# Kernel tuning notes

Measured on AMD Instinct MI355X. Metric: run time of the kernel, lower is better.

Reference implementation:

```python
import jax, jax.numpy as jnp
import numpy as np

N, C, H, W = 32, 512, 56, 56
L, CT, HEAD, GROUPS = 64, 512, 16, 16
SIZE, POS_DIM = 14, 49  # PosEncoder(size=14, num_downsample=1) -> 14^2 // 4 = 49


def setup_inputs() -> dict:
    key = jax.random.key(0)
    ks = jax.random.split(key, 8)
    return {
        "feature": jax.random.normal(ks[0], (N, C, H, W), jnp.float32),
        "w_tc": jax.random.normal(ks[1], (L, C), jnp.float32) * 0.02,
        "b_tc": jnp.zeros((L,), jnp.float32),
        "w_val": jax.random.normal(ks[2], (GROUPS, CT // GROUPS, C // GROUPS), jnp.float32) * 0.02,
        "b_val": jnp.zeros((CT,), jnp.float32),
        "w_ds3": jax.random.normal(ks[3], (1, 1, 3, 3), jnp.float32) * 0.1,
        "b_ds3": jnp.zeros((1,), jnp.float32),
        "w_ds1": jax.random.normal(ks[4], (1, 1), jnp.float32) * 0.1,
        "b_ds1": jnp.zeros((1,), jnp.float32),
        "w_pos": jax.random.normal(ks[5], (POS_DIM, POS_DIM), jnp.float32) * 0.02,
        "b_pos": jnp.zeros((POS_DIM,), jnp.float32),
        "w_tok": jax.random.normal(ks[6], (CT, CT + POS_DIM), jnp.float32) * 0.02,
        "b_tok": jnp.zeros((CT,), jnp.float32),
    }


def reference(feature, w_tc, b_tc, w_val, b_val, w_ds3, b_ds3, w_ds1, b_ds1,
              w_pos, b_pos, w_tok, b_tok):
    n, c, h, w = feature.shape
    hw = h * w
    # --- static token coefficients: 1x1 conv C->L, scale, softmax over HW ---
    tc = jnp.einsum('nchw,lc->nlhw', feature, w_tc) + b_tc[None, :, None, None]
    tc = tc.reshape(n, 1, L, hw).transpose(0, 1, 3, 2) / np.sqrt(c)  # (N,1,HW,L)
    tc = jax.nn.softmax(tc, axis=2)
    # --- grouped 1x1 conv value: C -> CT (groups=16) ---
    fg = feature.reshape(n, GROUPS, c // GROUPS, hw)
    val = jnp.einsum('ngci,gdc->ngdi', fg, w_val).reshape(n, CT, hw) + b_val[None, :, None]
    val = val.reshape(n, HEAD, CT // HEAD, hw)
    # --- token aggregation: (N,h,CT/h,HW) @ (N,1,HW,L) -> (N,CT,L) ---
    tokens = jnp.matmul(val, tc).reshape(n, CT, -1)
    # --- PosEncoder: view coef maps as images, nearest-resize to 14x14 ---
    pc = tc.reshape(n * L, 1, h, w)  # torch .view memory reinterpretation
    ih = (jnp.arange(SIZE) * h) // SIZE
    iw = (jnp.arange(SIZE) * w) // SIZE
    pc = pc[:, :, ih][:, :, :, iw]  # (N*L,1,14,14) nearest interpolate
    # conv3x3 stride 2 pad 1: 14 -> 7
    pc = jax.lax.conv_general_dilated(pc, w_ds3, (2, 2), ((1, 1), (1, 1))) + b_ds3[None, :, None, None]
    # conv1x1 (1->1)
    pc = jnp.einsum('nchw,dc->ndhw', pc, w_ds1) + b_ds1[None, :, None, None]
    pc = pc.reshape(n, L, POS_DIM).transpose(0, 2, 1)  # (N,49,L)
    pos = jnp.einsum('ncl,dc->ndl', pc, w_pos) + b_pos[None, :, None]
    # --- concat + final 1x1 conv1d (CT+49 -> CT) ---
    tokens = jnp.concatenate([tokens, pos], axis=1)
    tokens = jnp.einsum('ncl,dc->ndl', tokens, w_tok) + b_tok[None, :, None]
    return tokens  # (N, CT, L)
```

## Files before the change

### kernel.cpp

```cpp
#include <hip/hip_runtime.h>
#include <hip/hip_bf16.h>
#include <cstddef>
#include <cstdint>

namespace {

constexpr int kN = 32;
constexpr int kC = 512;
constexpr int kHW = 3136;
constexpr int kL = 64;
constexpr int kCT = 512;
constexpr int kTok = 561;
constexpr int kKcat = 576;

typedef float fx4 __attribute__((ext_vector_type(4)));
typedef float f32x4 __attribute__((ext_vector_type(4)));
typedef short short8 __attribute__((ext_vector_type(8)));
typedef unsigned int u32x2 __attribute__((ext_vector_type(2)));

static __device__ inline unsigned short bf16_1(float x) {
  __hip_bfloat16 h = __float2bfloat16(x);
  unsigned short u;
  __builtin_memcpy(&u, &h, 2);
  return u;
}
static __device__ inline unsigned pk2(float a, float b) {
  __hip_bfloat162 h2 = __float22bfloat162_rn(make_float2(a, b));
  unsigned u;
  __builtin_memcpy(&u, &h2, 4);
  return u;
}
static __device__ inline float bf2f(unsigned short h) {
  unsigned u = (unsigned)h << 16;
  float f;
  __builtin_memcpy(&f, &u, 4);
  return f;
}

__global__ __launch_bounds__(256) void prep_kernel(
    const float* __restrict__ w_tok, const float* __restrict__ w_val,
    const float* __restrict__ b_val, const float* __restrict__ b_tok,
    const float* __restrict__ w_tc, unsigned short* __restrict__ wcat16,
    float* __restrict__ cst, unsigned short* __restrict__ wtc16,
    float* __restrict__ denom, unsigned short* __restrict__ bcat16) {
  int idx = blockIdx.x * 256 + threadIdx.x;
  if (idx < kCT * kKcat) {
    int d = idx / kKcat;
    int c = idx - d * kKcat;
    float v = 0.f;
    if (c < kCT) {
      int g = c >> 5, k = c & 31;
      const float* wt = w_tok + (size_t)d * kTok + g * 32;
      const float* wv = w_val + g * 1024 + k;
      float s = 0.f;
#pragma unroll
      for (int dp = 0; dp < 32; ++dp) s += wt[dp] * wv[dp * 32];
      v = s;
    } else if (c < kTok) {
      v = w_tok[(size_t)d * kTok + c];
    }
    wcat16[idx] = bf16_1(v);
    return;
  }
  idx -= kCT * kKcat;
  if (idx < kCT) {
    float s = b_tok[idx];
    for (int c = 0; c < kCT; ++c) s += w_tok[(size_t)idx * kTok + c] * b_val[c];
    cst[idx] = s;
    return;
  }
  idx -= kCT;
  if (idx < kL * kC) {
    wtc16[idx] = bf16_1(w_tc[idx]);
    return;
  }
  idx -= kL * kC;
  if (idx < kN * kL) {
    denom[idx] = 0.f;
    return;
  }
  idx -= kN * kL;
  if (idx < kN * kL * 15) {
    int n = idx / (kL * 15);
    int r = idx - n * (kL * 15);
    int l = r / 15;
    int k = kTok + (r - l * 15);
    bcat16[(size_t)n * kL * kKcat + (size_t)l * kKcat + k] = 0;
  }
}

__global__ __launch_bounds__(256) void tc_gemm2_kernel(
    const float* __restrict__ feat, const unsigned short* __restrict__ wtc16,
    const float* __restrict__ b_tc, unsigned short* __restrict__ expT,
    unsigned short* __restrict__ feat16, float* __restrict__ denom) {
  const int n = blockIdx.y;
  const int pb = blockIdx.x * 128;
  const int tid = threadIdx.x;
  const int wave = tid >> 6, lane = tid & 63;
  const int quad = lane >> 4, l16 = lane & 15;
  __shared__ unsigned short Bs[128][72];
  __shared__ float bsm[64];
  __shared__ float denom_s[64];
  if (tid < 64) {
    bsm[tid] = b_tc[tid];
    denom_s[tid] = 0.f;
  }

  f32x4 acc[4][2];
#pragma unroll
  for (int i = 0; i < 4; ++i)
#pragma unroll
    for (int j = 0; j < 2; ++j) acc[i][j] = (f32x4){0.f, 0.f, 0.f, 0.f};

  const float* fb = feat + (size_t)n * kC * kHW;
  unsigned short* f16b = feat16 + (size_t)n * kC * kHW;
  const int bc4 = (tid & 15) * 4, bpl0 = (tid >> 4) * 4;
  int pe_[2];
#pragma unroll
  for (int pass = 0; pass < 2; ++pass) {
    int pe = pb + bpl0 + pass * 64;
    pe_[pass] = pe < 3132 ? pe : 3132;
  }

  fx4 va[2][4], vb[2][4];
  auto LOADT = [&](int c0, fx4 (&v)[2][4]) {
#pragma unroll
    for (int pass = 0; pass < 2; ++pass) {
      const float* s = fb + (size_t)(c0 + bc4) * kHW + pe_[pass];
#pragma unroll
      for (int r = 0; r < 4; ++r) v[pass][r] = *(const fx4*)(s + (size_t)r * kHW);
    }
  };
  auto STORET = [&](int c0, fx4 (&v)[2][4]) {
#pragma unroll
    for (int pass = 0; pass < 2; ++pass) {
      int base = bpl0 + pass * 64;
#pragma unroll
      for (int j = 0; j < 4; ++j) {
        u32x2 w = {pk2(v[pass][0][j], v[pass][1][j]),
                   pk2(v[pass][2][j], v[pass][3][j])};
        *(u32x2*)&Bs[base + j][bc4] = w;
      }
#pragma unroll
      for (int r = 0; r < 4; ++r) {
        u32x2 wf = {pk2(v[pass][r][0], v[pass][r][1]),
                    pk2(v[pass][r][2], v[pass][r][3])};
        *(u32x2*)(f16b + (size_t)(c0 + bc4 + r) * kHW + pe_[pass]) = wf;
      }
    }
  };
  auto COMPUTE = [&](int c0) {
#pragma unroll
    for (int ks = 0; ks < 2; ++ks) {
      short8 a[4], b[2];
#pragma unroll
      for (int i = 0; i < 4; ++i)
        a[i] = *(const short8*)(wtc16 + (size_t)(i * 16 + l16) * kC + c0 +
                                ks * 32 + quad * 8);
#pragma unroll
      for (int j = 0; j < 2; ++j)
        b[j] = *(const short8*)&Bs[wave * 32 + j * 16 + l16][ks * 32 + quad * 8];
#pragma unroll
      for (int i = 0; i < 4; ++i)
#pragma unroll
        for (int j = 0; j < 2; ++j)
          acc[i][j] = __builtin_amdgcn_mfma_f32_16x16x32_bf16(a[i], b[j],
                                                              acc[i][j], 0, 0, 0);
    }
  };

  LOADT(0, va);
#pragma unroll
  for (int c0 = 0; c0 < kC; c0 += 128) {
    STORET(c0, va);
    __syncthreads();
    LOADT(c0 + 64, vb);
    COMPUTE(c0);
    __syncthreads();
    STORET(c0 + 64, vb);
    __syncthreads();
    if (c0 + 128 < kC) LOADT(c0 + 128, va);
    COMPUTE(c0 + 64);
    __syncthreads();
  }

  const float inv = 0.04419417382415922f;
  unsigned short* eb = expT + (size_t)n * kL * kHW;
  float dsum[4][4];
#pragma unroll
  for (int ti = 0; ti < 4; ++ti)
#pragma unroll
    for (int r = 0; r < 4; ++r) dsum[ti][r] = 0.f;

#pragma unroll
  for (int ti = 0; ti < 4; ++ti) {
#pragma unroll
    for (int tj = 0; tj < 2; ++tj) {
      int pg = pb + wave * 32 + tj * 16 + l16;
      bool ok = pg < kHW;
#pragma unroll
      for (int r = 0; r < 4; ++r) {
        int l = ti * 16 + quad * 4 + r;
        float e = 0.f;
        if (ok) {
          float raw = (acc[ti][tj][r] + bsm[l]) * inv;
          unsigned short h = bf16_1(__expf(raw));
          eb[(size_t)l * kHW + pg] = h;
          e = bf2f(h);
        }
        dsum[ti][r] += e;
      }
    }
  }
#pragma unroll
  for (int off = 1; off < 16; off <<= 1) {
#pragma unroll
    for (int ti = 0; ti < 4; ++ti)
#pragma unroll
      for (int r = 0; r < 4; ++r) dsum[ti][r] += __shfl_xor(dsum[ti][r], off);
  }
  if (l16 == 0) {
#pragma unroll
    for (int ti = 0; ti < 4; ++ti)
#pragma unroll
      for (int r = 0; r < 4; ++r)
        atomicAdd(&denom_s[ti * 16 + quad * 4 + r], dsum[ti][r]);
  }
  __syncthreads();
  if (tid < 64) atomicAdd(&denom[n * 64 + tid], denom_s[tid]);
}

__global__ __launch_bounds__(256) void m_gemm3_kernel(
    const unsigned short* __restrict__ expT,
    const unsigned short* __restrict__ feat16, float* __restrict__ part,
    int klen) {
  const int cb = blockIdx.x * 256;
  const int n = blockIdx.y;
  const int s = blockIdx.z;
  const int p0s = s * klen;
  const int tid = threadIdx.x;
  const int wave = tid >> 6, lane = tid & 63;
  const int quad = lane >> 4, l16 = lane & 15;

  f32x4 acc[4][4];
#pragma unroll
  for (int i = 0; i < 4; ++i)
#pragma unroll
    for (int j = 0; j < 4; ++j) acc[i][j] = (f32x4){0.f, 0.f, 0.f, 0.f};

  const unsigned short* ea =
      expT + (size_t)n * kL * kHW + (size_t)l16 * kHW + quad * 8;
  const unsigned short* fbb =
      feat16 + (size_t)n * kC * kHW +
      (size_t)(cb + wave * 64 + l16) * kHW + quad * 8;

  auto LOAD = [&](int p0, short8 (&a)[4], short8 (&b)[4]) {
#pragma unroll
    for (int i = 0; i < 4; ++i)
      a[i] = *(const short8*)(ea + (size_t)i * 16 * kHW + p0);
#pragma unroll
    for (int j = 0; j < 4; ++j)
      b[j] = *(const short8*)(fbb + (size_t)j * 16 * kHW + p0);
  };
  auto MF = [&](short8 (&a)[4], short8 (&b)[4]) {
#pragma unroll
    for (int i = 0; i < 4; ++i)
#pragma unroll
      for (int j = 0; j < 4; ++j)
        acc[i][j] =
            __builtin_amdgcn_mfma_f32_16x16x32_bf16(a[i], b[j], acc[i][j], 0, 0, 0);
  };

  short8 aA[4], bA[4], aB[4], bB[4];
  const int nk = klen >> 5;
  LOAD(p0s, aA, bA);
  for (int t = 0; t < nk; t += 2) {
    const int p0 = p0s + t * 32;
    const bool m1 = (t + 1) < nk;
    if (m1) LOAD(p0 + 32, aB, bB);
    MF(aA, bA);
    if (m1) {
      if (t + 2 < nk) LOAD(p0 + 64, aA, bA);
      MF(aB, bB);
    }
  }

  float* ob = part + (size_t)(s * kN + n) * kL * kCT;
#pragma unroll
  for (int ti = 0; ti < 4; ++ti) {
#pragma unroll
    for (int tj = 0; tj < 4; ++tj) {
      int cg = cb + wave * 64 + tj * 16 + l16;
#pragma unroll
      for (int r = 0; r < 4; ++r) {
        int l = ti * 16 + quad * 4 + r;
        ob[(size_t)l * kCT + cg] = acc[ti][tj][r];
      }
    }
  }
}

__global__ __launch_bounds__(256) void reduce_pos_kernel(
    const float* __restrict__ part, const float* __restrict__ denom,
    unsigned short* __restrict__ bcat16, const unsigned short* __restrict__ expT,
    const float* __restrict__ w3, const float* __restrict__ b3,
    const float* __restrict__ w1, const float* __restrict__ b1,
    float* __restrict__ pcl, int ksplit) {
  int idx = blockIdx.x * 256 + threadIdx.x;
  if (idx < kN * kL * kCT) {
    int n = idx >> 15;
    int r = idx & 32767;
    int l = r >> 9;
    int c = r & 511;
    float s = 0.f;
    for (int ss = 0; ss < ksplit; ++ss)
      s += part[(size_t)ss * (kN * kL * kCT) + idx];
    float si = 1.f / denom[n * 64 + l];
    bcat16[(size_t)n * kL * kKcat + (size_t)l * kKcat + c] = bf16_1(s * si);
    return;
  }
  idx -= kN * kL * kCT;
  if (idx >= kN * kL * 49) return;
  int n = idx / (kL * 49);
  int r = idx - n * (kL * 49);
  int lp = r / 49;
  int o = r - lp * 49;
  int y = o / 7, x = o - y * 7;
  const unsigned short* eb = expT + (size_t)n * kL * kHW;
  const float* dB = denom + n * 64;
  float a = 0.f;
#pragma unroll
  for (int dy = 0; dy < 3; ++dy) {
    int i = 2 * y - 1 + dy;
    if (i < 0 || i >= 14) continue;
#pragma unroll
    for (int dx = 0; dx < 3; ++dx) {
      int j = 2 * x - 1 + dx;
      if (j < 0 || j >= 14) continue;
      int t = 224 * i + 4 * j;
      int lsm = t & 63;
      int p = lp * 49 + (t >> 6);
      float e = bf2f(eb[(size_t)lsm * kHW + p]);
      a += w3[dy * 3 + dx] * (e / dB[lsm]);
    }
  }
  pcl[(size_t)n * kL * 49 + lp * 49 + o] = (a + b3[0]) * w1[0] + b1[0];
}

__global__ __launch_bounds__(256) void pos_out2_kernel(
    const float* __restrict__ pcl, const float* __restrict__ wp,
    const float* __restrict__ bp, unsigned short* __restrict__ bcat16) {
  const int n = blockIdx.x;
  __shared__ float t[64 * 49];
  for (int i = threadIdx.x; i < 64 * 49; i += 256)
    t[i] = pcl[(size_t)n * 64 * 49 + i];
  __syncthreads();
  for (int o = threadIdx.x; o < 64 * 49; o += 256) {
    int l = o / 49, d = o - l * 49;
    float s = bp[d];
#pragma unroll 7
    for (int q = 0; q < 49; ++q) s += wp[d * 49 + q] * t[l * 49 + q];
    bcat16[(size_t)n * kL * kKcat + (size_t)l * kKcat + kCT + d] = bf16_1(s);
  }
}

__global__ __launch_bounds__(256) void out_gemm2_kernel(
    const unsigned short* __restrict__ wcat16,
    const unsigned short* __restrict__ bcat16, const float* __restrict__ cst,
    float* __restrict__ out) {
  const int db = blockIdx.x * 64;
  const int n = blockIdx.y;
  const int tid = threadIdx.x;
  const int wave = tid >> 6, lane = tid & 63;
  const int quad = lane >> 4, l16 = lane & 15;
  __shared__ float csm[64];
  if (tid < 64) csm[tid] = cst[db + tid];
  __syncthreads();

  f32x4 acc[4];
#pragma unroll
  for (int j = 0; j < 4; ++j) acc[j] = (f32x4){0.f, 0.f, 0.f, 0.f};

  const unsigned short* ab = wcat16 + (size_t)(db + wave * 16 + l16) * kKcat;
  const unsigned short* bb = bcat16 + (size_t)n * kL * kKcat;
#pragma unroll
  for (int k0 = 0; k0 < kKcat; k0 += 32) {
    short8 a = *(const short8*)(ab + k0 + quad * 8);
    short8 b[4];
#pragma unroll
    for (int j = 0; j < 4; ++j)
      b[j] = *(const short8*)(bb + (size_t)(j * 16 + l16) * kKcat + k0 + quad * 8);
#pragma unroll
    for (int j = 0; j < 4; ++j)
      acc[j] = __builtin_amdgcn_mfma_f32_16x16x32_bf16(a, b[j], acc[j], 0, 0, 0);
  }

  float* ob = out + (size_t)n * kCT * kL;
#pragma unroll
  for (int tj = 0; tj < 4; ++tj) {
    int lg = tj * 16 + l16;
#pragma unroll
    for (int r = 0; r < 4; ++r) {
      int dl = wave * 16 + quad * 4 + r;
      ob[(size_t)(db + dl) * kL + lg] = acc[tj][r] + csm[dl];
    }
  }
}

}

extern "C" void kernel_launch(void* const* d_in, const int* in_sizes, int n_in,
                              void* d_out, int out_size, void* d_ws,
                              size_t ws_size, hipStream_t stream) {
  (void)in_sizes; (void)n_in; (void)out_size;
  const float* feat  = (const float*)d_in[0];
  const float* w_tc  = (const float*)d_in[1];
  const float* b_tc  = (const float*)d_in[2];
  const float* w_val = (const float*)d_in[3];
  const float* b_val = (const float*)d_in[4];
  const float* w_ds3 = (const float*)d_in[5];
  const float* b_ds3 = (const float*)d_in[6];
  const float* w_ds1 = (const float*)d_in[7];
  const float* b_ds1 = (const float*)d_in[8];
  const float* w_pos = (const float*)d_in[9];
  const float* b_pos = (const float*)d_in[10];
  const float* w_tok = (const float*)d_in[11];
  const float* b_tok = (const float*)d_in[12];
  float* out = (float*)d_out;

  float* ws = (float*)d_ws;
  size_t off = 0;
  unsigned short* expT = (unsigned short*)(ws + off);   off += (size_t)kN * kL * kHW / 2;
  unsigned short* bcat16 = (unsigned short*)(ws + off); off += (size_t)kN * kL * kKcat / 2;
  unsigned short* wcat16 = (unsigned short*)(ws + off); off += (size_t)kCT * kKcat / 2;
  unsigned short* wtc16 = (unsigned short*)(ws + off);  off += (size_t)kL * kC / 2;
  float* cst = ws + off;   off += kCT;
  float* denom = ws + off; off += kN * kL;
  float* pcl = ws + off;   off += (size_t)kN * kL * 49;
  unsigned short* feat16 = (unsigned short*)(ws + off); off += (size_t)kN * kC * kHW / 2;
  float* part = ws + off;

  int ksplit = 14;
  if (ws_size < (off + (size_t)14 * kN * kL * kCT) * sizeof(float)) ksplit = 7;
  if (ws_size < (off + (size_t)7 * kN * kL * kCT) * sizeof(float)) ksplit = 1;
  const int klen = kHW / ksplit;

  prep_kernel<<<1410, 256, 0, stream>>>(w_tok, w_val, b_val, b_tok, w_tc,
                                        wcat16, cst, wtc16, denom, bcat16);
  tc_gemm2_kernel<<<dim3(25, kN), 256, 0, stream>>>(feat, wtc16, b_tc, expT,
                                                    feat16, denom);
  m_gemm3_kernel<<<dim3(2, kN, ksplit), 256, 0, stream>>>(expT, feat16, part,
                                                          klen);
  reduce_pos_kernel<<<4488, 256, 0, stream>>>(part, denom, bcat16, expT, w_ds3,
                                              b_ds3, w_ds1, b_ds1, pcl, ksplit);
  pos_out2_kernel<<<kN, 256, 0, stream>>>(pcl, w_pos, b_pos, bcat16);
  out_gemm2_kernel<<<dim3(8, kN), 256, 0, stream>>>(wcat16, bcat16, cst, out);
}
```

Baseline: 468.6 us.

## Split fp32-to-bf16 conversion into standalone kernel and narrow m_gemm channel tile

The fp32 to bf16 conversion of the feature map moves out of the coefficient GEMM into a separate streaming kernel. The coefficient GEMM now reads bf16 data and transposes it into shared memory with byte-permute instructions. The value-aggregation GEMM halves its channel tile per block (128 instead of 256), doubling the grid for more parallelism. A ksplit=2 fallback is also added. The cost is an extra kernel launch and an extra bf16 read of the feature map, in exchange for a simpler conversion path and higher occupancy.

After: 482.4 us. +3.0%, slower.

```diff
diff --git a/kernel.cpp b/kernel.cpp
--- a/kernel.cpp
+++ b/kernel.cpp
@@ -17,6 +17,7 @@
 typedef float f32x4 __attribute__((ext_vector_type(4)));
 typedef short short8 __attribute__((ext_vector_type(8)));
 typedef unsigned int u32x2 __attribute__((ext_vector_type(2)));
+typedef unsigned int u32x4 __attribute__((ext_vector_type(4)));
 
 static __device__ inline unsigned short bf16_1(float x) {
   __hip_bfloat16 h = __float2bfloat16(x);
@@ -89,10 +90,21 @@
   }
 }
 
-__global__ __launch_bounds__(256) void tc_gemm2_kernel(
-    const float* __restrict__ feat, const unsigned short* __restrict__ wtc16,
-    const float* __restrict__ b_tc, unsigned short* __restrict__ expT,
-    unsigned short* __restrict__ feat16, float* __restrict__ denom) {
+__global__ __launch_bounds__(256) void convert_kernel(
+    const float* __restrict__ feat, unsigned short* __restrict__ feat16) {
+  size_t idx = (size_t)blockIdx.x * 256 + threadIdx.x;
+  const float* s = feat + idx * 8;
+  fx4 v0 = *(const fx4*)s;
+  fx4 v1 = *(const fx4*)(s + 4);
+  u32x4 w = {pk2(v0[0], v0[1]), pk2(v0[2], v0[3]), pk2(v1[0], v1[1]),
+             pk2(v1[2], v1[3])};
+  *(u32x4*)(feat16 + idx * 8) = w;
+}
+
+__global__ __launch_bounds__(256) void tc_gemm3_kernel(
+    const unsigned short* __restrict__ feat16,
+    const unsigned short* __restrict__ wtc16, const float* __restrict__ b_tc,
+    unsigned short* __restrict__ expT, float* __restrict__ denom) {
   const int n = blockIdx.y;
   const int pb = blockIdx.x * 128;
   const int tid = threadIdx.x;
@@ -112,8 +124,7 @@
 #pragma unroll
     for (int j = 0; j < 2; ++j) acc[i][j] = (f32x4){0.f, 0.f, 0.f, 0.f};
 
-  const float* fb = feat + (size_t)n * kC * kHW;
-  unsigned short* f16b = feat16 + (size_t)n * kC * kHW;
+  const unsigned short* f16b = feat16 + (size_t)n * kC * kHW;
   const int bc4 = (tid & 15) * 4, bpl0 = (tid >> 4) * 4;
   int pe_[2];
 #pragma unroll
@@ -122,31 +133,32 @@
     pe_[pass] = pe < 3132 ? pe : 3132;
   }
 
-  fx4 va[2][4], vb[2][4];
-  auto LOADT = [&](int c0, fx4 (&v)[2][4]) {
+  u32x2 va[2][4], vb[2][4];
+  auto LOADT = [&](int c0, u32x2 (&v)[2][4]) {
 #pragma unroll
     for (int pass = 0; pass < 2; ++pass) {
-      const float* s = fb + (size_t)(c0 + bc4) * kHW + pe_[pass];
-#pragma unroll
-      for (int r = 0; r < 4; ++r) v[pass][r] = *(const fx4*)(s + (size_t)r * kHW);
+      const unsigned short* s = f16b + (size_t)(c0 + bc4) * kHW + pe_[pass];
+#pragma unroll
+      for (int r = 0; r < 4; ++r)
+        v[pass][r] = *(const u32x2*)(s + (size_t)r * kHW);
     }
   };
-  auto STORET = [&](int c0, fx4 (&v)[2][4]) {
+  auto STORET = [&](u32x2 (&v)[2][4]) {
 #pragma unroll
     for (int pass = 0; pass < 2; ++pass) {
       int base = bpl0 + pass * 64;
-#pragma unroll
-      for (int j = 0; j < 4; ++j) {
-        u32x2 w = {pk2(v[pass][0][j], v[pass][1][j]),
-                   pk2(v[pass][2][j], v[pass][3][j])};
-        *(u32x2*)&Bs[base + j][bc4] = w;
-      }
-#pragma unroll
-      for (int r = 0; r < 4; ++r) {
-        u32x2 wf = {pk2(v[pass][r][0], v[pass][r][1]),
-                    pk2(v[pass][r][2], v[pass][r][3])};
-        *(u32x2*)(f16b + (size_t)(c0 + bc4 + r) * kHW + pe_[pass]) = wf;
-      }
+      u32x2 o0 = {__builtin_amdgcn_perm(v[pass][1].x, v[pass][0].x, 0x05040100u),
+                  __builtin_amdgcn_perm(v[pass][3].x, v[pass][2].x, 0x05040100u)};
+      *(u32x2*)&Bs[base + 0][bc4] = o0;
+      u32x2 o1 = {__builtin_amdgcn_perm(v[pass][1].x, v[pass][0].x, 0x07060302u),
+                  __builtin_amdgcn_perm(v[pass][3].x, v[pass][2].x, 0x07060302u)};
+      *(u32x2*)&Bs[base + 1][bc4] = o1;
+      u32x2 o2 = {__builtin_amdgcn_perm(v[pass][1].y, v[pass][0].y, 0x05040100u),
+                  __builtin_amdgcn_perm(v[pass][3].y, v[pass][2].y, 0x05040100u)};
+      *(u32x2*)&Bs[base + 2][bc4] = o2;
+      u32x2 o3 = {__builtin_amdgcn_perm(v[pass][1].y, v[pass][0].y, 0x07060302u),
+                  __builtin_amdgcn_perm(v[pass][3].y, v[pass][2].y, 0x07060302u)};
+      *(u32x2*)&Bs[base + 3][bc4] = o3;
     }
   };
   auto COMPUTE = [&](int c0) {
@@ -172,12 +184,12 @@
   LOADT(0, va);
 #pragma unroll
   for (int c0 = 0; c0 < kC; c0 += 128) {
-    STORET(c0, va);
+    STORET(va);
     __syncthreads();
     LOADT(c0 + 64, vb);
     COMPUTE(c0);
     __syncthreads();
-    STORET(c0 + 64, vb);
+    STORET(vb);
     __syncthreads();
     if (c0 + 128 < kC) LOADT(c0 + 128, va);
     COMPUTE(c0 + 64);
@@ -230,11 +242,11 @@
   if (tid < 64) atomicAdd(&denom[n * 64 + tid], denom_s[tid]);
 }
 
-__global__ __launch_bounds__(256) void m_gemm3_kernel(
+__global__ __launch_bounds__(256) void m_gemm4_kernel(
     const unsigned short* __restrict__ expT,
     const unsigned short* __restrict__ feat16, float* __restrict__ part,
     int klen) {
-  const int cb = blockIdx.x * 256;
+  const int cb = blockIdx.x * 128;
   const int n = blockIdx.y;
   const int s = blockIdx.z;
   const int p0s = s * klen;
@@ -242,36 +254,36 @@
   const int wave = tid >> 6, lane = tid & 63;
   const int quad = lane >> 4, l16 = lane & 15;
 
-  f32x4 acc[4][4];
+  f32x4 acc[4][2];
 #pragma unroll
   for (int i = 0; i < 4; ++i)
 #pragma unroll
-    for (int j = 0; j < 4; ++j) acc[i][j] = (f32x4){0.f, 0.f, 0.f, 0.f};
+    for (int j = 0; j < 2; ++j) acc[i][j] = (f32x4){0.f, 0.f, 0.f, 0.f};
 
   const unsigned short* ea =
       expT + (size_t)n * kL * kHW + (size_t)l16 * kHW + quad * 8;
   const unsigned short* fbb =
-      feat16 + (size_t)n * kC * kHW +
-      (size_t)(cb + wave * 64 + l16) * kHW + quad * 8;
-
-  auto LOAD = [&](int p0, short8 (&a)[4], short8 (&b)[4]) {
+      feat16 + (size_t)n * kC * kHW + (size_t)(cb + wave * 32 + l16) * kHW +
+      quad * 8;
+
+  auto LOAD = [&](int p0, short8 (&a)[4], short8 (&b)[2]) {
 #pragma unroll
     for (int i = 0; i < 4; ++i)
       a[i] = *(const short8*)(ea + (size_t)i * 16 * kHW + p0);
 #pragma unroll
-    for (int j = 0; j < 4; ++j)
+    for (int j = 0; j < 2; ++j)
       b[j] = *(const short8*)(fbb + (size_t)j * 16 * kHW + p0);
   };
-  auto MF = [&](short8 (&a)[4], short8 (&b)[4]) {
+  auto MF = [&](short8 (&a)[4], short8 (&b)[2]) {
 #pragma unroll
     for (int i = 0; i < 4; ++i)
 #pragma unroll
-      for (int j = 0; j < 4; ++j)
+      for (int j = 0; j < 2; ++j)
         acc[i][j] =
             __builtin_amdgcn_mfma_f32_16x16x32_bf16(a[i], b[j], acc[i][j], 0, 0, 0);
   };
 
-  short8 aA[4], bA[4], aB[4], bB[4];
+  short8 aA[4], bA[2], aB[4], bB[2];
   const int nk = klen >> 5;
   LOAD(p0s, aA, bA);
   for (int t = 0; t < nk; t += 2) {
@@ -289,8 +301,8 @@
 #pragma unroll
   for (int ti = 0; ti < 4; ++ti) {
 #pragma unroll
-    for (int tj = 0; tj < 4; ++tj) {
-      int cg = cb + wave * 64 + tj * 16 + l16;
+    for (int tj = 0; tj < 2; ++tj) {
+      int cg = cb + wave * 32 + tj * 16 + l16;
 #pragma unroll
       for (int r = 0; r < 4; ++r) {
         int l = ti * 16 + quad * 4 + r;
@@ -442,14 +454,16 @@
 
   int ksplit = 14;
   if (ws_size < (off + (size_t)14 * kN * kL * kCT) * sizeof(float)) ksplit = 7;
-  if (ws_size < (off + (size_t)7 * kN * kL * kCT) * sizeof(float)) ksplit = 1;
+  if (ws_size < (off + (size_t)7 * kN * kL * kCT) * sizeof(float)) ksplit = 2;
+  if (ws_size < (off + (size_t)2 * kN * kL * kCT) * sizeof(float)) ksplit = 1;
   const int klen = kHW / ksplit;
 
   prep_kernel<<<1410, 256, 0, stream>>>(w_tok, w_val, b_val, b_tok, w_tc,
                                         wcat16, cst, wtc16, denom, bcat16);
-  tc_gemm2_kernel<<<dim3(25, kN), 256, 0, stream>>>(feat, wtc16, b_tc, expT,
-                                                    feat16, denom);
-  m_gemm3_kernel<<<dim3(2, kN, ksplit), 256, 0, stream>>>(expT, feat16, part,
+  convert_kernel<<<25088, 256, 0, stream>>>(feat, feat16);
+  tc_gemm3_kernel<<<dim3(25, kN), 256, 0, stream>>>(feat16, wtc16, b_tc, expT,
+                                                    denom);
+  m_gemm4_kernel<<<dim3(4, kN, ksplit), 256, 0, stream>>>(expT, feat16, part,
                                                           klen);
   reduce_pos_kernel<<<4488, 256, 0, stream>>>(part, denom, bcat16, expT, w_ds3,
                                               b_ds3, w_ds1, b_ds1, pcl, ksplit);
```

## Drop bf16 feature copy; convert fp32 feature on the fly in aggregation GEMM

Applied to the files above, without the earlier changes.

The coefficient GEMM no longer writes a bf16 copy of the feature tensor. The aggregation GEMM instead loads fp32 feature directly and packs it to bf16 in registers before MFMA. Tiles are narrowed to 128 channels and the split-K factor is halved to keep the block count, which also shrinks the partial buffer reduced afterwards. This trades a large global write plus reread for a wider fp32 read and extra conversion ALU work.

New measurement: 438.6 us. 1.07x faster.

```diff
diff --git a/kernel.cpp b/kernel.cpp
--- a/kernel.cpp
+++ b/kernel.cpp
@@ -17,6 +17,7 @@
 typedef float f32x4 __attribute__((ext_vector_type(4)));
 typedef short short8 __attribute__((ext_vector_type(8)));
 typedef unsigned int u32x2 __attribute__((ext_vector_type(2)));
+typedef unsigned int u32x4 __attribute__((ext_vector_type(4)));
 
 static __device__ inline unsigned short bf16_1(float x) {
   __hip_bfloat16 h = __float2bfloat16(x);
@@ -89,10 +90,10 @@
   }
 }
 
-__global__ __launch_bounds__(256) void tc_gemm2_kernel(
+__global__ __launch_bounds__(256) void tc_gemm4_kernel(
     const float* __restrict__ feat, const unsigned short* __restrict__ wtc16,
     const float* __restrict__ b_tc, unsigned short* __restrict__ expT,
-    unsigned short* __restrict__ feat16, float* __restrict__ denom) {
+    float* __restrict__ denom) {
   const int n = blockIdx.y;
   const int pb = blockIdx.x * 128;
   const int tid = threadIdx.x;
@@ -113,7 +114,6 @@
     for (int j = 0; j < 2; ++j) acc[i][j] = (f32x4){0.f, 0.f, 0.f, 0.f};
 
   const float* fb = feat + (size_t)n * kC * kHW;
-  unsigned short* f16b = feat16 + (size_t)n * kC * kHW;
   const int bc4 = (tid & 15) * 4, bpl0 = (tid >> 4) * 4;
   int pe_[2];
 #pragma unroll
@@ -131,7 +131,7 @@
       for (int r = 0; r < 4; ++r) v[pass][r] = *(const fx4*)(s + (size_t)r * kHW);
     }
   };
-  auto STORET = [&](int c0, fx4 (&v)[2][4]) {
+  auto STORET = [&](fx4 (&v)[2][4]) {
 #pragma unroll
     for (int pass = 0; pass < 2; ++pass) {
       int base = bpl0 + pass * 64;
@@ -141,12 +141,6 @@
                    pk2(v[pass][2][j], v[pass][3][j])};
         *(u32x2*)&Bs[base + j][bc4] = w;
       }
-#pragma unroll
-      for (int r = 0; r < 4; ++r) {
-        u32x2 wf = {pk2(v[pass][r][0], v[pass][r][1]),
-                    pk2(v[pass][r][2], v[pass][r][3])};
-        *(u32x2*)(f16b + (size_t)(c0 + bc4 + r) * kHW + pe_[pass]) = wf;
-      }
     }
   };
   auto COMPUTE = [&](int c0) {
@@ -172,12 +166,12 @@
   LOADT(0, va);
 #pragma unroll
   for (int c0 = 0; c0 < kC; c0 += 128) {
-    STORET(c0, va);
+    STORET(va);
     __syncthreads();
     LOADT(c0 + 64, vb);
     COMPUTE(c0);
     __syncthreads();
-    STORET(c0 + 64, vb);
+    STORET(vb);
     __syncthreads();
     if (c0 + 128 < kC) LOADT(c0 + 128, va);
     COMPUTE(c0 + 64);
@@ -230,11 +224,10 @@
   if (tid < 64) atomicAdd(&denom[n * 64 + tid], denom_s[tid]);
 }
 
-__global__ __launch_bounds__(256) void m_gemm3_kernel(
-    const unsigned short* __restrict__ expT,
-    const unsigned short* __restrict__ feat16, float* __restrict__ part,
-    int klen) {
-  const int cb = blockIdx.x * 256;
+__global__ __launch_bounds__(256) void m_gemm5_kernel(
+    const unsigned short* __restrict__ expT, const float* __restrict__ feat,
+    float* __restrict__ part, int klen) {
+  const int cb = blockIdx.x * 128;
   const int n = blockIdx.y;
   const int s = blockIdx.z;
   const int p0s = s * klen;
@@ -242,46 +235,65 @@
   const int wave = tid >> 6, lane = tid & 63;
   const int quad = lane >> 4, l16 = lane & 15;
 
-  f32x4 acc[4][4];
+  f32x4 acc[4][2];
 #pragma unroll
   for (int i = 0; i < 4; ++i)
 #pragma unroll
-    for (int j = 0; j < 4; ++j) acc[i][j] = (f32x4){0.f, 0.f, 0.f, 0.f};
+    for (int j = 0; j < 2; ++j) acc[i][j] = (f32x4){0.f, 0.f, 0.f, 0.f};
 
   const unsigned short* ea =
       expT + (size_t)n * kL * kHW + (size_t)l16 * kHW + quad * 8;
-  const unsigned short* fbb =
-      feat16 + (size_t)n * kC * kHW +
-      (size_t)(cb + wave * 64 + l16) * kHW + quad * 8;
-
-  auto LOAD = [&](int p0, short8 (&a)[4], short8 (&b)[4]) {
+  const float* fbb = feat + (size_t)n * kC * kHW +
+                     (size_t)(cb + wave * 32 + l16) * kHW + quad * 8;
+
+  auto LOADA = [&](int p0, short8 (&a)[4]) {
 #pragma unroll
     for (int i = 0; i < 4; ++i)
       a[i] = *(const short8*)(ea + (size_t)i * 16 * kHW + p0);
-#pragma unroll
-    for (int j = 0; j < 4; ++j)
-      b[j] = *(const short8*)(fbb + (size_t)j * 16 * kHW + p0);
-  };
-  auto MF = [&](short8 (&a)[4], short8 (&b)[4]) {
+  };
+  auto LOADB = [&](int p0, fx4 (&bf)[2][2]) {
+#pragma unroll
+    for (int j = 0; j < 2; ++j) {
+      const float* src = fbb + (size_t)j * 16 * kHW + p0;
+      bf[j][0] = *(const fx4*)src;
+      bf[j][1] = *(const fx4*)(src + 4);
+    }
+  };
+  auto CVTMF = [&](short8 (&a)[4], fx4 (&bf)[2][2]) {
+    short8 b[2];
+#pragma unroll
+    for (int j = 0; j < 2; ++j) {
+      u32x4 w = {pk2(bf[j][0][0], bf[j][0][1]), pk2(bf[j][0][2], bf[j][0][3]),
+                 pk2(bf[j][1][0], bf[j][1][1]), pk2(bf[j][1][2], bf[j][1][3])};
+      __builtin_memcpy(&b[j], &w, 16);
+    }
 #pragma unroll
     for (int i = 0; i < 4; ++i)
 #pragma unroll
-      for (int j = 0; j < 4; ++j)
+      for (int j = 0; j < 2; ++j)
         acc[i][j] =
             __builtin_amdgcn_mfma_f32_16x16x32_bf16(a[i], b[j], acc[i][j], 0, 0, 0);
   };
 
-  short8 aA[4], bA[4], aB[4], bB[4];
+  short8 aA[4], aB[4];
+  fx4 fA[2][2], fB[2][2];
   const int nk = klen >> 5;
-  LOAD(p0s, aA, bA);
+  LOADA(p0s, aA);
+  LOADB(p0s, fA);
   for (int t = 0; t < nk; t += 2) {
     const int p0 = p0s + t * 32;
     const bool m1 = (t + 1) < nk;
-    if (m1) LOAD(p0 + 32, aB, bB);
-    MF(aA, bA);
     if (m1) {
-      if (t + 2 < nk) LOAD(p0 + 64, aA, bA);
-      MF(aB, bB);
+      LOADA(p0 + 32, aB);
+      LOADB(p0 + 32, fB);
+    }
+    CVTMF(aA, fA);
+    if (m1) {
+      if (t + 2 < nk) {
+        LOADA(p0 + 64, aA);
+        LOADB(p0 + 64, fA);
+      }
+      CVTMF(aB, fB);
     }
   }
 
@@ -289,8 +301,8 @@
 #pragma unroll
   for (int ti = 0; ti < 4; ++ti) {
 #pragma unroll
-    for (int tj = 0; tj < 4; ++tj) {
-      int cg = cb + wave * 64 + tj * 16 + l16;
+    for (int tj = 0; tj < 2; ++tj) {
+      int cg = cb + wave * 32 + tj * 16 + l16;
 #pragma unroll
       for (int r = 0; r < 4; ++r) {
         int l = ti * 16 + quad * 4 + r;
@@ -437,19 +449,18 @@
   float* cst = ws + off;   off += kCT;
   float* denom = ws + off; off += kN * kL;
   float* pcl = ws + off;   off += (size_t)kN * kL * 49;
-  unsigned short* feat16 = (unsigned short*)(ws + off); off += (size_t)kN * kC * kHW / 2;
   float* part = ws + off;
 
-  int ksplit = 14;
-  if (ws_size < (off + (size_t)14 * kN * kL * kCT) * sizeof(float)) ksplit = 7;
-  if (ws_size < (off + (size_t)7 * kN * kL * kCT) * sizeof(float)) ksplit = 1;
+  int ksplit = 7;
+  if (ws_size < (off + (size_t)7 * kN * kL * kCT) * sizeof(float)) ksplit = 2;
+  if (ws_size < (off + (size_t)2 * kN * kL * kCT) * sizeof(float)) ksplit = 1;
   const int klen = kHW / ksplit;
 
   prep_kernel<<<1410, 256, 0, stream>>>(w_tok, w_val, b_val, b_tok, w_tc,
                                         wcat16, cst, wtc16, denom, bcat16);
-  tc_gemm2_kernel<<<dim3(25, kN), 256, 0, stream>>>(feat, wtc16, b_tc, expT,
-                                                    feat16, denom);
-  m_gemm3_kernel<<<dim3(2, kN, ksplit), 256, 0, stream>>>(expT, feat16, part,
+  tc_gemm4_kernel<<<dim3(25, kN), 256, 0, stream>>>(feat, wtc16, b_tc, expT,
+                                                    denom);
+  m_gemm5_kernel<<<dim3(4, kN, ksplit), 256, 0, stream>>>(expT, feat, part,
                                                           klen);
   reduce_pos_kernel<<<4488, 256, 0, stream>>>(part, denom, bcat16, expT, w_ds3,
                                               b_ds3, w_ds1, b_ds1, pcl, ksplit);
```
